# Optimization experiments

Measured on AMD Instinct MI355X. Metric: run time of the kernel, lower is better.

## Reference

```python
import jax, jax.numpy as jnp
import numpy as np

S = 64.0
MARGIN = 0.5

def setup_inputs() -> dict:
    key = jax.random.key(0)
    k1, k2 = jax.random.split(key)
    B, C = 256, 100000
    # cosine similarities in (-0.99, 0.99) so arccos is well-conditioned
    logits = jax.random.uniform(k1, (B, C), dtype=jnp.float32, minval=-0.99, maxval=0.99)
    labels = jax.random.randint(k2, (B,), 0, C, dtype=jnp.int64)
    return {"logits": logits, "labels": labels}

def _arcface(logits, labels):
    B = logits.shape[0]
    valid = labels != -1                     # rows with a real target
    safe_labels = jnp.where(valid, labels, 0)
    rows = jnp.arange(B)
    target = logits[rows, safe_labels]       # [B] target cosines
    # original does arccos over the whole matrix then cos back; off-target
    # entries reduce to identity, targets become cos(arccos(x) + m)
    new_target = jnp.cos(jnp.arccos(target) + MARGIN)
    new_target = jnp.where(valid, new_target, target)
    modified = logits.at[rows, safe_labels].set(new_target)
    # the no_grad block + custom Function make backward exactly grad * s
    return S * (logits + jax.lax.stop_gradient(modified - logits))

def reference(logits, labels):
    return _arcface(logits, labels)
```

## Files before the change

### kernel.cpp

```cpp
#include <hip/hip_runtime.h>
#include <hip/hip_bf16.h>
#include <math.h>


#define ARC_S      64.0f
#define COS_M      0.8775825618903728f
#define SIN_M      0.4794255386042030f

typedef float floatx4 __attribute__((ext_vector_type(4)));

__global__ __launch_bounds__(256) void scale_copy_kernel(
    const floatx4* __restrict__ in,
    floatx4*       __restrict__ out)
{
    const size_t base = (size_t)blockIdx.x * 2048u + threadIdx.x;

    floatx4 v[8];
    #pragma unroll
    for (int j = 0; j < 8; ++j)
        v[j] = in[base + j * 256];

    __builtin_amdgcn_sched_barrier(0);

    #pragma unroll
    for (int j = 0; j < 8; ++j)
        out[base + j * 256] = v[j] * ARC_S;
}

__global__ __launch_bounds__(256) void fixup_kernel(
    const float* __restrict__ logits,
    const int*   __restrict__ labels,
    float*       __restrict__ out,
    int B, int C, size_t tailStart, size_t total)
{
    const int t = threadIdx.x;

    if (t < B) {
        const int lbl = labels[t];
        if (lbl >= 0 && lbl < C) {
            const size_t idx = (size_t)t * (size_t)C + (size_t)lbl;
            const float x = logits[idx];
            const float s = sqrtf(fmaxf(0.0f, 1.0f - x * x));
            out[idx] = ARC_S * (x * COS_M - s * SIN_M);
        }
    }

    for (size_t i = tailStart + t; i < total; i += 256)
        out[i] = ARC_S * logits[i];
}

extern "C" void kernel_launch(void* const* d_in, const int* in_sizes, int n_in,
                              void* d_out, int out_size, void* d_ws, size_t ws_size,
                              hipStream_t stream) {
    const float* logits = (const float*)d_in[0];
    const int*   labels = (const int*)d_in[1];
    float*       out    = (float*)d_out;

    const int B = in_sizes[1];
    const int C = in_sizes[0] / B;
    const size_t total  = (size_t)B * (size_t)C;
    const size_t total4 = total / 4;
    const int    nChunks = (int)(total4 / 2048);
    const size_t tailStart = (size_t)nChunks * 2048u * 4u;

    scale_copy_kernel<<<dim3(nChunks), dim3(256), 0, stream>>>(
        (const floatx4*)logits, (floatx4*)out);
    fixup_kernel<<<dim3(1), dim3(256), 0, stream>>>(
        logits, labels, out, B, C, tailStart, total);
}
```

Before: 182.0 us.

## Split scale-copy into grid-synchronized read phase and write phase

Adds a cooperative kernel in which each thread first loads 32 float4 values into registers, then waits at a grid-wide barrier before storing the scaled values, with a strided loop covering whatever remains. The aim is to keep DRAM reads and writes from interleaving across the whole device, cutting read/write turnaround. The cost is the overlap between reads and writes, plus a grid-sync and cooperative-launch overhead and heavy register use. When cooperative launch is not possible, it falls back to a grid-stride version of the old copy kernel with a separate tail kernel.

```diff
diff --git a/kernel.cpp b/kernel.cpp
--- a/kernel.cpp
+++ b/kernel.cpp
@@ -1,6 +1,8 @@
 #include <hip/hip_runtime.h>
-#include <hip/hip_bf16.h>
+#include <hip/hip_cooperative_groups.h>
 #include <math.h>
+
+namespace cg = cooperative_groups;
 
 
 #define ARC_S      64.0f
@@ -9,22 +11,58 @@
 
 typedef float floatx4 __attribute__((ext_vector_type(4)));
 
+#define PHASE_NB   768
+#define PHASE_NT   256
+#define PER_THREAD 32
+
+__global__ __launch_bounds__(PHASE_NT, 3) void phased_copy_kernel(
+    const floatx4* __restrict__ in,
+    floatx4*       __restrict__ out,
+    size_t total4)
+{
+    const size_t stride = (size_t)PHASE_NB * PHASE_NT;
+    const size_t gtid   = (size_t)blockIdx.x * PHASE_NT + threadIdx.x;
+
+    floatx4 v[PER_THREAD];
+    #pragma unroll
+    for (int k = 0; k < PER_THREAD; ++k)
+        v[k] = in[gtid + (size_t)k * stride];
+
+    cg::this_grid().sync();
+
+    #pragma unroll
+    for (int k = 0; k < PER_THREAD; ++k)
+        out[gtid + (size_t)k * stride] = v[k] * ARC_S;
+
+    for (size_t i = (size_t)PER_THREAD * stride + gtid; i < total4; i += stride)
+        out[i] = in[i] * ARC_S;
+}
+
 __global__ __launch_bounds__(256) void scale_copy_kernel(
     const floatx4* __restrict__ in,
-    floatx4*       __restrict__ out)
+    floatx4*       __restrict__ out,
+    int nUnits)
 {
-    const size_t base = (size_t)blockIdx.x * 2048u + threadIdx.x;
+    const int t = threadIdx.x;
+    for (int bu = blockIdx.x; bu < nUnits; bu += gridDim.x) {
+        const size_t base = (size_t)bu * 2048u + (size_t)t;
+        floatx4 v[8];
+        #pragma unroll
+        for (int j = 0; j < 8; ++j)
+            v[j] = in[base + j * 256];
+        #pragma unroll
+        for (int j = 0; j < 8; ++j)
+            out[base + j * 256] = v[j] * ARC_S;
+    }
+}
 
-    floatx4 v[8];
-    #pragma unroll
-    for (int j = 0; j < 8; ++j)
-        v[j] = in[base + j * 256];
-
-    __builtin_amdgcn_sched_barrier(0);
-
-    #pragma unroll
-    for (int j = 0; j < 8; ++j)
-        out[base + j * 256] = v[j] * ARC_S;
+__global__ __launch_bounds__(256) void tail_copy_kernel(
+    const float* __restrict__ in, float* __restrict__ out,
+    size_t start, size_t total)
+{
+    for (size_t i = start + threadIdx.x + (size_t)blockIdx.x * 256u;
+         i < total; i += (size_t)gridDim.x * 256u)
+        out[i] = ARC_S * in[i];
 }
 
 __global__ __launch_bounds__(256) void fixup_kernel(
@@ -60,11 +98,41 @@
     const int C = in_sizes[0] / B;
     const size_t total  = (size_t)B * (size_t)C;
     const size_t total4 = total / 4;
-    const int    nChunks = (int)(total4 / 2048);
-    const size_t tailStart = (size_t)nChunks * 2048u * 4u;
+    const size_t vecTail = total4 * 4;
 
-    scale_copy_kernel<<<dim3(nChunks), dim3(256), 0, stream>>>(
-        (const floatx4*)logits, (floatx4*)out);
+    static int coopOK = -1;
+    if (coopOK < 0) {
+        int dev = 0;
+        hipGetDevice(&dev);
+        hipDeviceProp_t prop;
+        hipGetDeviceProperties(&prop, dev);
+        int perCU = 0;
+        hipOccupancyMaxActiveBlocksPerMultiprocessor(
+            &perCU, (const void*)phased_copy_kernel, PHASE_NT, 0);
+        coopOK = ((long long)perCU * prop.multiProcessorCount >= PHASE_NB &&
+                  prop.cooperativeLaunch) ? 1 : 0;
+    }
+
+    const size_t phaseCover = (size_t)PHASE_NB * PHASE_NT * PER_THREAD;
+
+    if (coopOK == 1 && total4 >= phaseCover) {
+        void* args[] = { (void*)&logits, (void*)&out, (void*)&total4 };
+        hipLaunchCooperativeKernel((const void*)phased_copy_kernel,
+                                   dim3(PHASE_NB), dim3(PHASE_NT),
+                                   args, 0, stream);
+    } else {
+        const int nUnits = (int)(total4 / 2048);
+        if (nUnits > 0) {
+            const int nBlocks = nUnits < 2048 ? nUnits : 2048;
+            scale_copy_kernel<<<dim3(nBlocks), dim3(256), 0, stream>>>(
+                (const floatx4*)logits, (floatx4*)out, nUnits);
+        }
+        const size_t unitTail = (size_t)(total4 / 2048) * 2048u;
+        if (unitTail < total4)
+            tail_copy_kernel<<<dim3(64), dim3(256), 0, stream>>>(
+                logits, out, unitTail * 4u, vecTail);
+    }
+
     fixup_kernel<<<dim3(1), dim3(256), 0, stream>>>(
-        logits, labels, out, B, C, tailStart, total);
+        logits, labels, out, B, C, vecTail, total);
 }
```

Measured after the change: 183.4 us. No clear change (+0.7%).
